# Kernel tuning notes

Measured on AMD Instinct MI355X. Metric: run time of the kernel, lower is better.

Reference implementation:

```python
import jax, jax.numpy as jnp
import numpy as np

ROUTING_ITERS = 3

def squash(t, axis=-1):
    sq_norm = jnp.sum(t * t, axis=axis, keepdims=True)
    scale = sq_norm / (1.0 + sq_norm)
    return scale * t / jnp.sqrt(sq_norm + 1e-8)

def setup_inputs() -> dict:
    key = jax.random.key(0)
    k1, k2 = jax.random.split(key)
    B, N, I, J, O = 64, 2048, 16, 32, 32
    x = jax.random.normal(k1, (B, N, I), dtype=jnp.float32)
    weights = jax.random.normal(k2, (N, J, O, I), dtype=jnp.float32) * 0.1
    return {"x": x, "weights": weights}

def reference(x, weights):
    B, N, _ = x.shape
    J = weights.shape[1]
    # predictions u_{j|i}: [B, N, J, O]
    predictions = jnp.einsum('bni,njoi->bnjo', x, weights)
    b = jnp.zeros((B, N, J, 1), dtype=x.dtype)
    v = None
    for i in range(ROUTING_ITERS):
        c = jax.nn.softmax(b, axis=2)                      # coupling over capsules J
        s = jnp.sum(predictions * c, axis=1, keepdims=True)  # [B,1,J,O]
        v = squash(s, axis=-1)
        if i < ROUTING_ITERS - 1:
            agreement = jnp.sum(predictions * v, axis=-1, keepdims=True)  # [B,N,J,1]
            b = b + agreement
    return jnp.squeeze(v, axis=1)  # [B, J, O]
```

## Files before the change

kernel.cpp:

```cpp
#include <hip/hip_runtime.h>
#include <hip/hip_bf16.h>

#define B_ 64
#define N_ 2048
#define I_ 16
#define J_ 32
#define O_ 32
#define JO_ 1024
#define SPLITS 32

typedef __attribute__((ext_vector_type(8))) short bf16x8;
typedef __attribute__((ext_vector_type(16))) float f32x16;
typedef unsigned short u16;
typedef unsigned int u32;

__device__ __forceinline__ float bf2f(u16 u) {
  union { u32 i; float f; } c; c.i = ((u32)u) << 16; return c.f;
}
__device__ __forceinline__ u16 f2bf(float f) {
  union { float f; u32 i; } c; c.f = f;
  u32 r = (c.i + 0x7fffu + ((c.i >> 16) & 1u)) >> 16;
  return (u16)r;
}
__device__ __forceinline__ u32 pack2_pk(float lo, float hi) {
  u32 r;
  asm("v_cvt_pk_bf16_f32 %0, %1, %2" : "=v"(r) : "v"(lo), "v"(hi));
  return r;
}
__device__ __forceinline__ u32 scale2_pk(u32 p, float cv) {
  union { u32 i; float f; } lo, hi;
  lo.i = p << 16; hi.i = p & 0xffff0000u;
  return pack2_pk(lo.f * cv, hi.f * cv);
}

__global__ __launch_bounds__(256) void xconv_kernel(
    const float* __restrict__ xf, u16* __restrict__ xt)
{
  const int idx = blockIdx.x * 256 + threadIdx.x;
  const int b = idx >> 11, n = idx & 2047;
  const float4* sp = (const float4*)(xf + (size_t)idx * 16);
  float4 f0 = sp[0], f1 = sp[1], f2 = sp[2], f3 = sp[3];
  uint4 d0, d1;
  d0.x = pack2_pk(f0.x, f0.y); d0.y = pack2_pk(f0.z, f0.w);
  d0.z = pack2_pk(f1.x, f1.y); d0.w = pack2_pk(f1.z, f1.w);
  d1.x = pack2_pk(f2.x, f2.y); d1.y = pack2_pk(f2.z, f2.w);
  d1.z = pack2_pk(f3.x, f3.y); d1.w = pack2_pk(f3.z, f3.w);
  uint4* dp = (uint4*)(xt + ((size_t)n * 64 + b) * 16);
  dp[0] = d0; dp[1] = d1;
}

#define SF_NPW 16

__global__ __launch_bounds__(256, 4) void wsf_kernel(
    const float* __restrict__ wf, u16* __restrict__ wb,
    const u16* __restrict__ xt, float* __restrict__ s_part)
{
  __shared__ float red[4][2048];
  const int tid = threadIdx.x;
  const int wave = tid >> 6, lane = tid & 63;
  const int l31 = lane & 31, h = lane >> 5;
  const int j = blockIdx.x, split = blockIdx.y;
  const int n0 = (split * 4 + wave) * SF_NPW;
  f32x16 acc0 = {0.f, 0.f, 0.f, 0.f, 0.f, 0.f, 0.f, 0.f,
                 0.f, 0.f, 0.f, 0.f, 0.f, 0.f, 0.f, 0.f};
  f32x16 acc1 = acc0;

  #pragma unroll 4
  for (int i = 0; i < SF_NPW; ++i) {
    const int n = n0 + i;
    const size_t row = (size_t)n * JO_ + j * 32 + l31;
    const float* wsrc = wf + row * 16 + h * 8;
    const float4 f0 = *(const float4*)(wsrc);
    const float4 f1 = *(const float4*)(wsrc + 4);
    union { uint4 u4; bf16x8 bv; } wd;
    wd.u4.x = pack2_pk(f0.x, f0.y); wd.u4.y = pack2_pk(f0.z, f0.w);
    wd.u4.z = pack2_pk(f1.x, f1.y); wd.u4.w = pack2_pk(f1.z, f1.w);
    *(uint4*)(wb + row * 16 + h * 8) = wd.u4;
    const bf16x8 x0 = *(const bf16x8*)(xt + ((size_t)n * 64 + l31) * 16 + h * 8);
    const bf16x8 x1 = *(const bf16x8*)(xt + ((size_t)n * 64 + 32 + l31) * 16 + h * 8);
    acc0 = __builtin_amdgcn_mfma_f32_32x32x16_bf16(wd.bv, x0, acc0, 0, 0, 0);
    acc1 = __builtin_amdgcn_mfma_f32_32x32x16_bf16(wd.bv, x1, acc1, 0, 0, 0);
  }
  #pragma unroll
  for (int r = 0; r < 16; ++r) {
    const int o = (r & 3) + 8 * (r >> 2) + 4 * h;
    red[wave][o * 64 + l31] = acc0[r];
    red[wave][o * 64 + 32 + l31] = acc1[r];
  }
  __syncthreads();
  float* dst = s_part + (size_t)split * (JO_ * B_) + (size_t)j * 32 * 64;
  #pragma unroll
  for (int k = 0; k < 8; ++k) {
    const int idx = tid + 256 * k;
    dst[idx] = red[0][idx] + red[1][idx] + red[2][idx] + red[3][idx];
  }
}

__global__ __launch_bounds__(256, 4) void sf_kernel(
    const u16* __restrict__ xt, const u16* __restrict__ wb,
    const u16* __restrict__ ct, float* __restrict__ s_part)
{
  __shared__ float red[4][2048];
  const int tid = threadIdx.x;
  const int wave = tid >> 6, lane = tid & 63;
  const int l31 = lane & 31, h = lane >> 5;
  const int j = blockIdx.x, split = blockIdx.y;
  const int n0 = (split * 4 + wave) * SF_NPW;
  f32x16 acc0 = {0.f, 0.f, 0.f, 0.f, 0.f, 0.f, 0.f, 0.f,
                 0.f, 0.f, 0.f, 0.f, 0.f, 0.f, 0.f, 0.f};
  f32x16 acc1 = acc0;

  #pragma unroll 4
  for (int i = 0; i < SF_NPW; ++i) {
    const int n = n0 + i;
    bf16x8 wfr = *(const bf16x8*)(wb + ((size_t)n * JO_ + j * 32 + l31) * 16 + h * 8);
    union { bf16x8 v; u32 u[4]; } a, b2;
    a.v = *(const bf16x8*)(xt + ((size_t)n * 64 + l31) * 16 + h * 8);
    b2.v = *(const bf16x8*)(xt + ((size_t)n * 64 + 32 + l31) * 16 + h * 8);
    const float cv0 = bf2f(ct[((size_t)j * N_ + n) * 64 + l31]);
    const float cv1 = bf2f(ct[((size_t)j * N_ + n) * 64 + 32 + l31]);
    a.u[0] = scale2_pk(a.u[0], cv0); a.u[1] = scale2_pk(a.u[1], cv0);
    a.u[2] = scale2_pk(a.u[2], cv0); a.u[3] = scale2_pk(a.u[3], cv0);
    b2.u[0] = scale2_pk(b2.u[0], cv1); b2.u[1] = scale2_pk(b2.u[1], cv1);
    b2.u[2] = scale2_pk(b2.u[2], cv1); b2.u[3] = scale2_pk(b2.u[3], cv1);
    acc0 = __builtin_amdgcn_mfma_f32_32x32x16_bf16(wfr, a.v, acc0, 0, 0, 0);
    acc1 = __builtin_amdgcn_mfma_f32_32x32x16_bf16(wfr, b2.v, acc1, 0, 0, 0);
  }
  #pragma unroll
  for (int r = 0; r < 16; ++r) {
    const int o = (r & 3) + 8 * (r >> 2) + 4 * h;
    red[wave][o * 64 + l31] = acc0[r];
    red[wave][o * 64 + 32 + l31] = acc1[r];
  }
  __syncthreads();
  float* dst = s_part + (size_t)split * (JO_ * B_) + (size_t)j * 32 * 64;
  #pragma unroll
  for (int k = 0; k < 8; ++k) {
    const int idx = tid + 256 * k;
    dst[idx] = red[0][idx] + red[1][idx] + red[2][idx] + red[3][idx];
  }
}

__global__ __launch_bounds__(64) void r_kernel(
    const float* __restrict__ s_part, float* __restrict__ v,
    const float* __restrict__ vprev, u16* __restrict__ v4,
    float* __restrict__ out, int mode, float scale)
{
  const int tid = threadIdx.x;
  const int jj = tid >> 5, o = tid & 31;
  const int b = blockIdx.x >> 4, jg = blockIdx.x & 15;
  const int j = jg * 2 + jj;
  const size_t off_jo = (size_t)(j * 32 + o) * 64 + b;
  float s = 0.f;
  #pragma unroll
  for (int k = 0; k < SPLITS; ++k) s += s_part[(size_t)k * (JO_ * B_) + off_jo];
  s *= scale;
  float sq = s * s;
  #pragma unroll
  for (int m = 16; m >= 1; m >>= 1) sq += __shfl_xor(sq, m, 64);
  const float sc = sq / (1.f + sq) * rsqrtf(sq + 1e-8f);
  const float vv = sc * s;
  const size_t off = (size_t)b * JO_ + j * 32 + o;
  const int g = o >> 3, hh = (o >> 2) & 1, rr = o & 3;
  const size_t v4off = ((((size_t)j * 4 + g) * 2 + hh) * 64 + b) * 4 + rr;
  if (mode == 0) { v[off] = vv; v4[v4off] = f2bf(vv); }
  else if (mode == 1) { v4[v4off] = f2bf(vv + vprev[off]); }
  else { out[off] = vv; }
}

__global__ __launch_bounds__(256, 6) void a_kernel(
    const u16* __restrict__ xt, const u16* __restrict__ wb,
    const u16* __restrict__ v4, u16* __restrict__ ct)
{
  __shared__ float lgs[64][33];
  const int tid = threadIdx.x;
  const int wave = tid >> 6, lane = tid & 63;
  const int l31 = lane & 31, h = lane >> 5;
  const int n = blockIdx.x;
  const f32x16 zero16 = {0.f, 0.f, 0.f, 0.f, 0.f, 0.f, 0.f, 0.f,
                         0.f, 0.f, 0.f, 0.f, 0.f, 0.f, 0.f, 0.f};

  const bf16x8 x0 = *(const bf16x8*)(xt + ((size_t)n * 64 + l31) * 16 + h * 8);
  const bf16x8 x1 = *(const bf16x8*)(xt + ((size_t)n * 64 + 32 + l31) * 16 + h * 8);

  #pragma unroll 2
  for (int tt = 0; tt < 8; ++tt) {
    const int t = wave * 8 + tt;
    const bf16x8 wfr =
        *(const bf16x8*)(wb + ((size_t)n * JO_ + t * 32 + l31) * 16 + h * 8);
    f32x16 p0 = __builtin_amdgcn_mfma_f32_32x32x16_bf16(wfr, x0, zero16, 0, 0, 0);
    f32x16 p1 = __builtin_amdgcn_mfma_f32_32x32x16_bf16(wfr, x1, zero16, 0, 0, 0);
    float s0 = 0.f, s1 = 0.f;
    #pragma unroll
    for (int g = 0; g < 4; ++g) {
      const int vbase = (((t * 4 + g) * 2 + h) * 64) * 4;
      const ushort4 va = *(const ushort4*)(v4 + vbase + l31 * 4);
      const ushort4 vb = *(const ushort4*)(v4 + vbase + (32 + l31) * 4);
      s0 += p0[g * 4 + 0] * bf2f(va.x) + p0[g * 4 + 1] * bf2f(va.y)
          + p0[g * 4 + 2] * bf2f(va.z) + p0[g * 4 + 3] * bf2f(va.w);
      s1 += p1[g * 4 + 0] * bf2f(vb.x) + p1[g * 4 + 1] * bf2f(vb.y)
          + p1[g * 4 + 2] * bf2f(vb.z) + p1[g * 4 + 3] * bf2f(vb.w);
    }
    s0 += __shfl_xor(s0, 32, 64);
    s1 += __shfl_xor(s1, 32, 64);
    lgs[lane][t] = h ? s1 : s0;
  }
  __syncthreads();

  if (tid < 64) {
    const int b = tid;
    float lv[32];
    float mx = -1e30f;
    #pragma unroll
    for (int t = 0; t < 32; ++t) { lv[t] = lgs[b][t]; mx = fmaxf(mx, lv[t]); }
    float sm = 0.f;
    #pragma unroll
    for (int t = 0; t < 32; ++t) { lv[t] = __expf(lv[t] - mx); sm += lv[t]; }
    const float inv = 1.f / sm;
    #pragma unroll
    for (int t = 0; t < 32; ++t) lgs[b][t] = lv[t] * inv;
  }
  __syncthreads();

  #pragma unroll
  for (int k = 0; k < 8; ++k) {
    const int idx = k * 256 + tid;
    const int t = idx >> 6, b = idx & 63;
    ct[((size_t)t * N_ + n) * 64 + b] = f2bf(lgs[b][t]);
  }
}

extern "C" void kernel_launch(void* const* d_in, const int* in_sizes, int n_in,
                              void* d_out, int out_size, void* d_ws, size_t ws_size,
                              hipStream_t stream) {
  const float* x = (const float*)d_in[0];
  const float* w = (const float*)d_in[1];
  float* out = (float*)d_out;
  char* ws = (char*)d_ws;
  u16*   wb     = (u16*)ws;
  u16*   ct     = (u16*)(ws + (size_t)64 * 1024 * 1024);
  u16*   xt     = (u16*)(ws + (size_t)72 * 1024 * 1024);
  float* s_part = (float*)(ws + (size_t)76 * 1024 * 1024);
  float* v0     = (float*)(ws + (size_t)84 * 1024 * 1024);
  u16*   v4     = (u16*)(ws + (size_t)84 * 1024 * 1024 + 262144);

  dim3 sfg(32, SPLITS), sfb(256);
  dim3 ag(2048), ab(256);
  dim3 rg(1024), rb(64);

  xconv_kernel<<<dim3(512), dim3(256), 0, stream>>>(x, xt);
  wsf_kernel<<<sfg, sfb, 0, stream>>>(w, wb, xt, s_part);
  r_kernel<<<rg, rb, 0, stream>>>(s_part, v0, v0, v4, out, 0, 0.03125f);
  a_kernel<<<ag, ab, 0, stream>>>(xt, wb, v4, ct);
  sf_kernel<<<sfg, sfb, 0, stream>>>(xt, wb, ct, s_part);
  r_kernel<<<rg, rb, 0, stream>>>(s_part, v0, v0, v4, out, 1, 1.0f);
  a_kernel<<<ag, ab, 0, stream>>>(xt, wb, v4, ct);
  sf_kernel<<<sfg, sfb, 0, stream>>>(xt, wb, ct, s_part);
  r_kernel<<<rg, rb, 0, stream>>>(s_part, v0, v0, v4, out, 2, 1.0f);
}
```

Baseline: 331.0 us.

## Fuse agreement, softmax and weighted sum into one per-capsule-set kernel

Replaces the separate agreement/softmax kernel and the weighted-sum kernel with a single kernel. Each block handles 8 input capsules: it computes logits, applies softmax in shared memory, then reuses the same weight and x fragments for the coupled sum. This removes the round trip of the bf16 coupling tensor through global memory and one of the two full passes over the weights per routing iteration. In exchange it writes 256 fp32 partial sums of the full output per iteration. A new reduction kernel then has to read those partials back, which adds substantial memory traffic and an extra launch.

Result: slower. 344.2 us (+4.0%).

```diff
diff --git a/kernel.cpp b/kernel.cpp
--- a/kernel.cpp
+++ b/kernel.cpp
@@ -8,6 +8,8 @@
 #define O_ 32
 #define JO_ 1024
 #define SPLITS 32
+#define ASF_NSET 8
+#define ASF_BLOCKS (N_ / ASF_NSET)
 
 typedef __attribute__((ext_vector_type(8))) short bf16x8;
 typedef __attribute__((ext_vector_type(16))) float f32x16;
@@ -96,53 +98,123 @@
   }
 }
 
-__global__ __launch_bounds__(256, 4) void sf_kernel(
+__global__ __launch_bounds__(512, 2) void asf_kernel(
     const u16* __restrict__ xt, const u16* __restrict__ wb,
-    const u16* __restrict__ ct, float* __restrict__ s_part)
-{
-  __shared__ float red[4][2048];
+    const u16* __restrict__ v4, float* __restrict__ s_part)
+{
+  __shared__ float lgs[ASF_NSET][32][64];
   const int tid = threadIdx.x;
   const int wave = tid >> 6, lane = tid & 63;
   const int l31 = lane & 31, h = lane >> 5;
-  const int j = blockIdx.x, split = blockIdx.y;
-  const int n0 = (split * 4 + wave) * SF_NPW;
-  f32x16 acc0 = {0.f, 0.f, 0.f, 0.f, 0.f, 0.f, 0.f, 0.f,
-                 0.f, 0.f, 0.f, 0.f, 0.f, 0.f, 0.f, 0.f};
-  f32x16 acc1 = acc0;
-
-  #pragma unroll 4
-  for (int i = 0; i < SF_NPW; ++i) {
-    const int n = n0 + i;
-    bf16x8 wfr = *(const bf16x8*)(wb + ((size_t)n * JO_ + j * 32 + l31) * 16 + h * 8);
-    union { bf16x8 v; u32 u[4]; } a, b2;
-    a.v = *(const bf16x8*)(xt + ((size_t)n * 64 + l31) * 16 + h * 8);
-    b2.v = *(const bf16x8*)(xt + ((size_t)n * 64 + 32 + l31) * 16 + h * 8);
-    const float cv0 = bf2f(ct[((size_t)j * N_ + n) * 64 + l31]);
-    const float cv1 = bf2f(ct[((size_t)j * N_ + n) * 64 + 32 + l31]);
-    a.u[0] = scale2_pk(a.u[0], cv0); a.u[1] = scale2_pk(a.u[1], cv0);
-    a.u[2] = scale2_pk(a.u[2], cv0); a.u[3] = scale2_pk(a.u[3], cv0);
-    b2.u[0] = scale2_pk(b2.u[0], cv1); b2.u[1] = scale2_pk(b2.u[1], cv1);
-    b2.u[2] = scale2_pk(b2.u[2], cv1); b2.u[3] = scale2_pk(b2.u[3], cv1);
-    acc0 = __builtin_amdgcn_mfma_f32_32x32x16_bf16(wfr, a.v, acc0, 0, 0, 0);
-    acc1 = __builtin_amdgcn_mfma_f32_32x32x16_bf16(wfr, b2.v, acc1, 0, 0, 0);
-  }
-  #pragma unroll
-  for (int r = 0; r < 16; ++r) {
-    const int o = (r & 3) + 8 * (r >> 2) + 4 * h;
-    red[wave][o * 64 + l31] = acc0[r];
-    red[wave][o * 64 + 32 + l31] = acc1[r];
+  const int nbase = blockIdx.x * ASF_NSET;
+  const f32x16 zero16 = {0.f, 0.f, 0.f, 0.f, 0.f, 0.f, 0.f, 0.f,
+                         0.f, 0.f, 0.f, 0.f, 0.f, 0.f, 0.f, 0.f};
+
+  for (int nn = 0; nn < ASF_NSET; ++nn) {
+    const int n = nbase + nn;
+    const bf16x8 x0 = *(const bf16x8*)(xt + ((size_t)n * 64 + l31) * 16 + h * 8);
+    const bf16x8 x1 = *(const bf16x8*)(xt + ((size_t)n * 64 + 32 + l31) * 16 + h * 8);
+    #pragma unroll 2
+    for (int q = 0; q < 4; ++q) {
+      const int t = wave * 4 + q;
+      const bf16x8 wfr =
+          *(const bf16x8*)(wb + ((size_t)n * JO_ + t * 32 + l31) * 16 + h * 8);
+      f32x16 p0 = __builtin_amdgcn_mfma_f32_32x32x16_bf16(wfr, x0, zero16, 0, 0, 0);
+      f32x16 p1 = __builtin_amdgcn_mfma_f32_32x32x16_bf16(wfr, x1, zero16, 0, 0, 0);
+      float s0 = 0.f, s1 = 0.f;
+      #pragma unroll
+      for (int g = 0; g < 4; ++g) {
+        const int vbase = (((t * 4 + g) * 2 + h) * 64) * 4;
+        const ushort4 va = *(const ushort4*)(v4 + vbase + l31 * 4);
+        const ushort4 vb = *(const ushort4*)(v4 + vbase + (32 + l31) * 4);
+        s0 += p0[g * 4 + 0] * bf2f(va.x) + p0[g * 4 + 1] * bf2f(va.y)
+            + p0[g * 4 + 2] * bf2f(va.z) + p0[g * 4 + 3] * bf2f(va.w);
+        s1 += p1[g * 4 + 0] * bf2f(vb.x) + p1[g * 4 + 1] * bf2f(vb.y)
+            + p1[g * 4 + 2] * bf2f(vb.z) + p1[g * 4 + 3] * bf2f(vb.w);
+      }
+      s0 += __shfl_xor(s0, 32, 64);
+      s1 += __shfl_xor(s1, 32, 64);
+      lgs[nn][t][lane] = h ? s1 : s0;
+    }
   }
   __syncthreads();
-  float* dst = s_part + (size_t)split * (JO_ * B_) + (size_t)j * 32 * 64;
-  #pragma unroll
-  for (int k = 0; k < 8; ++k) {
-    const int idx = tid + 256 * k;
-    dst[idx] = red[0][idx] + red[1][idx] + red[2][idx] + red[3][idx];
-  }
+
+  {
+    const int n2 = tid >> 6, b = tid & 63;
+    float lv[32];
+    float mx = -1e30f;
+    #pragma unroll
+    for (int t = 0; t < 32; ++t) { lv[t] = lgs[n2][t][b]; mx = fmaxf(mx, lv[t]); }
+    float sm = 0.f;
+    #pragma unroll
+    for (int t = 0; t < 32; ++t) { lv[t] = __expf(lv[t] - mx); sm += lv[t]; }
+    const float inv = 1.f / sm;
+    #pragma unroll
+    for (int t = 0; t < 32; ++t) lgs[n2][t][b] = lv[t] * inv;
+  }
+  __syncthreads();
+
+  f32x16 a0_0 = zero16, a0_1 = zero16, a0_2 = zero16, a0_3 = zero16;
+  f32x16 a1_0 = zero16, a1_1 = zero16, a1_2 = zero16, a1_3 = zero16;
+  for (int nn = 0; nn < ASF_NSET; ++nn) {
+    const int n = nbase + nn;
+    union { bf16x8 v; u32 u[4]; } xa, xb;
+    xa.v = *(const bf16x8*)(xt + ((size_t)n * 64 + l31) * 16 + h * 8);
+    xb.v = *(const bf16x8*)(xt + ((size_t)n * 64 + 32 + l31) * 16 + h * 8);
+    #pragma unroll
+    for (int q = 0; q < 4; ++q) {
+      const int t = wave * 4 + q;
+      const bf16x8 wfr =
+          *(const bf16x8*)(wb + ((size_t)n * JO_ + t * 32 + l31) * 16 + h * 8);
+      const float cv0 = lgs[nn][t][l31];
+      const float cv1 = lgs[nn][t][32 + l31];
+      union { bf16x8 v; u32 u[4]; } s0, s1;
+      s0.u[0] = scale2_pk(xa.u[0], cv0); s0.u[1] = scale2_pk(xa.u[1], cv0);
+      s0.u[2] = scale2_pk(xa.u[2], cv0); s0.u[3] = scale2_pk(xa.u[3], cv0);
+      s1.u[0] = scale2_pk(xb.u[0], cv1); s1.u[1] = scale2_pk(xb.u[1], cv1);
+      s1.u[2] = scale2_pk(xb.u[2], cv1); s1.u[3] = scale2_pk(xb.u[3], cv1);
+      if (q == 0) {
+        a0_0 = __builtin_amdgcn_mfma_f32_32x32x16_bf16(wfr, s0.v, a0_0, 0, 0, 0);
+        a1_0 = __builtin_amdgcn_mfma_f32_32x32x16_bf16(wfr, s1.v, a1_0, 0, 0, 0);
+      } else if (q == 1) {
+        a0_1 = __builtin_amdgcn_mfma_f32_32x32x16_bf16(wfr, s0.v, a0_1, 0, 0, 0);
+        a1_1 = __builtin_amdgcn_mfma_f32_32x32x16_bf16(wfr, s1.v, a1_1, 0, 0, 0);
+      } else if (q == 2) {
+        a0_2 = __builtin_amdgcn_mfma_f32_32x32x16_bf16(wfr, s0.v, a0_2, 0, 0, 0);
+        a1_2 = __builtin_amdgcn_mfma_f32_32x32x16_bf16(wfr, s1.v, a1_2, 0, 0, 0);
+      } else {
+        a0_3 = __builtin_amdgcn_mfma_f32_32x32x16_bf16(wfr, s0.v, a0_3, 0, 0, 0);
+        a1_3 = __builtin_amdgcn_mfma_f32_32x32x16_bf16(wfr, s1.v, a1_3, 0, 0, 0);
+      }
+    }
+  }
+  float* dst = s_part + (size_t)blockIdx.x * (JO_ * B_);
+  #pragma unroll
+  for (int q = 0; q < 4; ++q) {
+    const int t = wave * 4 + q;
+    const f32x16 a0 = (q == 0) ? a0_0 : (q == 1) ? a0_1 : (q == 2) ? a0_2 : a0_3;
+    const f32x16 a1 = (q == 0) ? a1_0 : (q == 1) ? a1_1 : (q == 2) ? a1_2 : a1_3;
+    #pragma unroll
+    for (int r = 0; r < 16; ++r) {
+      const int o = (r & 3) + 8 * (r >> 2) + 4 * h;
+      dst[(size_t)(t * 32 + o) * 64 + l31] = a0[r];
+      dst[(size_t)(t * 32 + o) * 64 + 32 + l31] = a1[r];
+    }
+  }
+}
+
+__global__ __launch_bounds__(256) void rs_kernel(
+    const float* __restrict__ src, float* __restrict__ dst, int nsplit)
+{
+  const int idx = blockIdx.x * 256 + threadIdx.x;
+  float s = 0.f;
+  #pragma unroll 8
+  for (int p = 0; p < nsplit; ++p) s += src[(size_t)p * (JO_ * B_) + idx];
+  dst[idx] = s;
 }
 
 __global__ __launch_bounds__(64) void r_kernel(
-    const float* __restrict__ s_part, float* __restrict__ v,
+    const float* __restrict__ s_red, float* __restrict__ v,
     const float* __restrict__ vprev, u16* __restrict__ v4,
     float* __restrict__ out, int mode, float scale)
 {
@@ -150,11 +222,7 @@
   const int jj = tid >> 5, o = tid & 31;
   const int b = blockIdx.x >> 4, jg = blockIdx.x & 15;
   const int j = jg * 2 + jj;
-  const size_t off_jo = (size_t)(j * 32 + o) * 64 + b;
-  float s = 0.f;
-  #pragma unroll
-  for (int k = 0; k < SPLITS; ++k) s += s_part[(size_t)k * (JO_ * B_) + off_jo];
-  s *= scale;
+  const float s = s_red[(size_t)(j * 32 + o) * 64 + b] * scale;
   float sq = s * s;
   #pragma unroll
   for (int m = 16; m >= 1; m >>= 1) sq += __shfl_xor(sq, m, 64);
@@ -168,68 +236,6 @@
   else { out[off] = vv; }
 }
 
-__global__ __launch_bounds__(256, 6) void a_kernel(
-    const u16* __restrict__ xt, const u16* __restrict__ wb,
-    const u16* __restrict__ v4, u16* __restrict__ ct)
-{
-  __shared__ float lgs[64][33];
-  const int tid = threadIdx.x;
-  const int wave = tid >> 6, lane = tid & 63;
-  const int l31 = lane & 31, h = lane >> 5;
-  const int n = blockIdx.x;
-  const f32x16 zero16 = {0.f, 0.f, 0.f, 0.f, 0.f, 0.f, 0.f, 0.f,
-                         0.f, 0.f, 0.f, 0.f, 0.f, 0.f, 0.f, 0.f};
-
-  const bf16x8 x0 = *(const bf16x8*)(xt + ((size_t)n * 64 + l31) * 16 + h * 8);
-  const bf16x8 x1 = *(const bf16x8*)(xt + ((size_t)n * 64 + 32 + l31) * 16 + h * 8);
-
-  #pragma unroll 2
-  for (int tt = 0; tt < 8; ++tt) {
-    const int t = wave * 8 + tt;
-    const bf16x8 wfr =
-        *(const bf16x8*)(wb + ((size_t)n * JO_ + t * 32 + l31) * 16 + h * 8);
-    f32x16 p0 = __builtin_amdgcn_mfma_f32_32x32x16_bf16(wfr, x0, zero16, 0, 0, 0);
-    f32x16 p1 = __builtin_amdgcn_mfma_f32_32x32x16_bf16(wfr, x1, zero16, 0, 0, 0);
-    float s0 = 0.f, s1 = 0.f;
-    #pragma unroll
-    for (int g = 0; g < 4; ++g) {
-      const int vbase = (((t * 4 + g) * 2 + h) * 64) * 4;
-      const ushort4 va = *(const ushort4*)(v4 + vbase + l31 * 4);
-      const ushort4 vb = *(const ushort4*)(v4 + vbase + (32 + l31) * 4);
-      s0 += p0[g * 4 + 0] * bf2f(va.x) + p0[g * 4 + 1] * bf2f(va.y)
-          + p0[g * 4 + 2] * bf2f(va.z) + p0[g * 4 + 3] * bf2f(va.w);
-      s1 += p1[g * 4 + 0] * bf2f(vb.x) + p1[g * 4 + 1] * bf2f(vb.y)
-          + p1[g * 4 + 2] * bf2f(vb.z) + p1[g * 4 + 3] * bf2f(vb.w);
-    }
-    s0 += __shfl_xor(s0, 32, 64);
-    s1 += __shfl_xor(s1, 32, 64);
-    lgs[lane][t] = h ? s1 : s0;
-  }
-  __syncthreads();
-
-  if (tid < 64) {
-    const int b = tid;
-    float lv[32];
-    float mx = -1e30f;
-    #pragma unroll
-    for (int t = 0; t < 32; ++t) { lv[t] = lgs[b][t]; mx = fmaxf(mx, lv[t]); }
-    float sm = 0.f;
-    #pragma unroll
-    for (int t = 0; t < 32; ++t) { lv[t] = __expf(lv[t] - mx); sm += lv[t]; }
-    const float inv = 1.f / sm;
-    #pragma unroll
-    for (int t = 0; t < 32; ++t) lgs[b][t] = lv[t] * inv;
-  }
-  __syncthreads();
-
-  #pragma unroll
-  for (int k = 0; k < 8; ++k) {
-    const int idx = k * 256 + tid;
-    const int t = idx >> 6, b = idx & 63;
-    ct[((size_t)t * N_ + n) * 64 + b] = f2bf(lgs[b][t]);
-  }
-}
-
 extern "C" void kernel_launch(void* const* d_in, const int* in_sizes, int n_in,
                               void* d_out, int out_size, void* d_ws, size_t ws_size,
                               hipStream_t stream) {
@@ -237,24 +243,27 @@
   const float* w = (const float*)d_in[1];
   float* out = (float*)d_out;
   char* ws = (char*)d_ws;
-  u16*   wb     = (u16*)ws;
-  u16*   ct     = (u16*)(ws + (size_t)64 * 1024 * 1024);
-  u16*   xt     = (u16*)(ws + (size_t)72 * 1024 * 1024);
-  float* s_part = (float*)(ws + (size_t)76 * 1024 * 1024);
-  float* v0     = (float*)(ws + (size_t)84 * 1024 * 1024);
-  u16*   v4     = (u16*)(ws + (size_t)84 * 1024 * 1024 + 262144);
+  u16*   wb       = (u16*)ws;
+  u16*   xt       = (u16*)(ws + (size_t)64 * 1024 * 1024);
+  float* s_part32 = (float*)(ws + (size_t)68 * 1024 * 1024);
+  float* s_red    = (float*)(ws + (size_t)76 * 1024 * 1024);
+  float* v0       = (float*)(ws + (size_t)76 * 1024 * 1024 + 262144);
+  u16*   v4       = (u16*)(ws + (size_t)76 * 1024 * 1024 + 2 * 262144);
+  float* s_partA  = (float*)(ws + (size_t)80 * 1024 * 1024);
 
   dim3 sfg(32, SPLITS), sfb(256);
-  dim3 ag(2048), ab(256);
+  dim3 ag(ASF_BLOCKS), ab(512);
+  dim3 rsg(256), rsb(256);
   dim3 rg(1024), rb(64);
 
   xconv_kernel<<<dim3(512), dim3(256), 0, stream>>>(x, xt);
-  wsf_kernel<<<sfg, sfb, 0, stream>>>(w, wb, xt, s_part);
-  r_kernel<<<rg, rb, 0, stream>>>(s_part, v0, v0, v4, out, 0, 0.03125f);
-  a_kernel<<<ag, ab, 0, stream>>>(xt, wb, v4, ct);
-  sf_kernel<<<sfg, sfb, 0, stream>>>(xt, wb, ct, s_part);
-  r_kernel<<<rg, rb, 0, stream>>>(s_part, v0, v0, v4, out, 1, 1.0f);
-  a_kernel<<<ag, ab, 0, stream>>>(xt, wb, v4, ct);
-  sf_kernel<<<sfg, sfb, 0, stream>>>(xt, wb, ct, s_part);
-  r_kernel<<<rg, rb, 0, stream>>>(s_part, v0, v0, v4, out, 2, 1.0f);
-}
+  wsf_kernel<<<sfg, sfb, 0, stream>>>(w, wb, xt, s_part32);
+  rs_kernel<<<rsg, rsb, 0, stream>>>(s_part32, s_red, SPLITS);
+  r_kernel<<<rg, rb, 0, stream>>>(s_red, v0, v0, v4, out, 0, 0.03125f);
+  asf_kernel<<<ag, ab, 0, stream>>>(xt, wb, v4, s_partA);
+  rs_kernel<<<rsg, rsb, 0, stream>>>(s_partA, s_red, ASF_BLOCKS);
+  r_kernel<<<rg, rb, 0, stream>>>(s_red, v0, v0, v4, out, 1, 1.0f);
+  asf_kernel<<<ag, ab, 0, stream>>>(xt, wb, v4, s_partA);
+  rs_kernel<<<rsg, rsb, 0, stream>>>(s_partA, s_red, ASF_BLOCKS);
+  r_kernel<<<rg, rb, 0, stream>>>(s_red, v0, v0, v4, out, 2, 1.0f);
+}
```

## Software-pipeline sf/a loads, double sf splits, add coalesced split-reduction kernel

Applied to the files above, without the earlier changes.

The sf kernel now uses 64 splits of 8 rows each and prefetches the next row's W, x and coupling values one iteration ahead. The agreement kernel gets the same prefetch, and the v4 layout is reorganised so each lane reads 16 contiguous bf16 values as two uint4 loads. The split-partial summation moves out of r_kernel into a separate coalesced rs_kernel. The goal is to hide load latency and raise parallelism, at the cost of more partial-sum traffic and three extra launches.

Result: slower. 904.3 us (+173.2%).

```diff
diff --git a/kernel.cpp b/kernel.cpp
--- a/kernel.cpp
+++ b/kernel.cpp
@@ -7,7 +7,8 @@
 #define J_ 32
 #define O_ 32
 #define JO_ 1024
-#define SPLITS 32
+#define WSPLITS 32
+#define SFSPLITS 64
 
 typedef __attribute__((ext_vector_type(8))) short bf16x8;
 typedef __attribute__((ext_vector_type(16))) float f32x16;
@@ -31,6 +32,17 @@
   union { u32 i; float f; } lo, hi;
   lo.i = p << 16; hi.i = p & 0xffff0000u;
   return pack2_pk(lo.f * cv, hi.f * cv);
+}
+__device__ __forceinline__ float dot16(const f32x16& p, uint4 lo, uint4 hi) {
+  const u32 w[8] = {lo.x, lo.y, lo.z, lo.w, hi.x, hi.y, hi.z, hi.w};
+  float s = 0.f;
+  #pragma unroll
+  for (int k = 0; k < 8; ++k) {
+    union { u32 i; float f; } a, b;
+    a.i = w[k] << 16; b.i = w[k] & 0xffff0000u;
+    s += p[2 * k] * a.f + p[2 * k + 1] * b.f;
+  }
+  return s;
 }
 
 __global__ __launch_bounds__(256) void xconv_kernel(
@@ -49,7 +61,7 @@
   dp[0] = d0; dp[1] = d1;
 }
 
-#define SF_NPW 16
+#define WSF_NPW 16
 
 __global__ __launch_bounds__(256, 4) void wsf_kernel(
     const float* __restrict__ wf, u16* __restrict__ wb,
@@ -60,13 +72,13 @@
   const int wave = tid >> 6, lane = tid & 63;
   const int l31 = lane & 31, h = lane >> 5;
   const int j = blockIdx.x, split = blockIdx.y;
-  const int n0 = (split * 4 + wave) * SF_NPW;
+  const int n0 = (split * 4 + wave) * WSF_NPW;
   f32x16 acc0 = {0.f, 0.f, 0.f, 0.f, 0.f, 0.f, 0.f, 0.f,
                  0.f, 0.f, 0.f, 0.f, 0.f, 0.f, 0.f, 0.f};
   f32x16 acc1 = acc0;
 
   #pragma unroll 4
-  for (int i = 0; i < SF_NPW; ++i) {
+  for (int i = 0; i < WSF_NPW; ++i) {
     const int n = n0 + i;
     const size_t row = (size_t)n * JO_ + j * 32 + l31;
     const float* wsrc = wf + row * 16 + h * 8;
@@ -96,6 +108,8 @@
   }
 }
 
+#define SF_NPW 8
+
 __global__ __launch_bounds__(256, 4) void sf_kernel(
     const u16* __restrict__ xt, const u16* __restrict__ wb,
     const u16* __restrict__ ct, float* __restrict__ s_part)
@@ -110,21 +124,35 @@
                  0.f, 0.f, 0.f, 0.f, 0.f, 0.f, 0.f, 0.f};
   f32x16 acc1 = acc0;
 
-  #pragma unroll 4
+  bf16x8 wfr = *(const bf16x8*)(wb + ((size_t)n0 * JO_ + j * 32 + l31) * 16 + h * 8);
+  union { bf16x8 v; u32 u[4]; } xa, xb;
+  xa.v = *(const bf16x8*)(xt + ((size_t)n0 * 64 + l31) * 16 + h * 8);
+  xb.v = *(const bf16x8*)(xt + ((size_t)n0 * 64 + 32 + l31) * 16 + h * 8);
+  float cv0 = bf2f(ct[((size_t)j * N_ + n0) * 64 + l31]);
+  float cv1 = bf2f(ct[((size_t)j * N_ + n0) * 64 + 32 + l31]);
+
+  #pragma unroll
   for (int i = 0; i < SF_NPW; ++i) {
-    const int n = n0 + i;
-    bf16x8 wfr = *(const bf16x8*)(wb + ((size_t)n * JO_ + j * 32 + l31) * 16 + h * 8);
-    union { bf16x8 v; u32 u[4]; } a, b2;
-    a.v = *(const bf16x8*)(xt + ((size_t)n * 64 + l31) * 16 + h * 8);
-    b2.v = *(const bf16x8*)(xt + ((size_t)n * 64 + 32 + l31) * 16 + h * 8);
-    const float cv0 = bf2f(ct[((size_t)j * N_ + n) * 64 + l31]);
-    const float cv1 = bf2f(ct[((size_t)j * N_ + n) * 64 + 32 + l31]);
-    a.u[0] = scale2_pk(a.u[0], cv0); a.u[1] = scale2_pk(a.u[1], cv0);
-    a.u[2] = scale2_pk(a.u[2], cv0); a.u[3] = scale2_pk(a.u[3], cv0);
-    b2.u[0] = scale2_pk(b2.u[0], cv1); b2.u[1] = scale2_pk(b2.u[1], cv1);
-    b2.u[2] = scale2_pk(b2.u[2], cv1); b2.u[3] = scale2_pk(b2.u[3], cv1);
-    acc0 = __builtin_amdgcn_mfma_f32_32x32x16_bf16(wfr, a.v, acc0, 0, 0, 0);
-    acc1 = __builtin_amdgcn_mfma_f32_32x32x16_bf16(wfr, b2.v, acc1, 0, 0, 0);
+    bf16x8 wfr_n = wfr;
+    union { bf16x8 v; u32 u[4]; } xa_n, xb_n;
+    xa_n.v = xa.v; xb_n.v = xb.v;
+    float c0n = cv0, c1n = cv1;
+    if (i + 1 < SF_NPW) {
+      const int n1 = n0 + i + 1;
+      wfr_n = *(const bf16x8*)(wb + ((size_t)n1 * JO_ + j * 32 + l31) * 16 + h * 8);
+      xa_n.v = *(const bf16x8*)(xt + ((size_t)n1 * 64 + l31) * 16 + h * 8);
+      xb_n.v = *(const bf16x8*)(xt + ((size_t)n1 * 64 + 32 + l31) * 16 + h * 8);
+      c0n = bf2f(ct[((size_t)j * N_ + n1) * 64 + l31]);
+      c1n = bf2f(ct[((size_t)j * N_ + n1) * 64 + 32 + l31]);
+    }
+    union { bf16x8 v; u32 u[4]; } s0, s1;
+    s0.u[0] = scale2_pk(xa.u[0], cv0); s0.u[1] = scale2_pk(xa.u[1], cv0);
+    s0.u[2] = scale2_pk(xa.u[2], cv0); s0.u[3] = scale2_pk(xa.u[3], cv0);
+    s1.u[0] = scale2_pk(xb.u[0], cv1); s1.u[1] = scale2_pk(xb.u[1], cv1);
+    s1.u[2] = scale2_pk(xb.u[2], cv1); s1.u[3] = scale2_pk(xb.u[3], cv1);
+    acc0 = __builtin_amdgcn_mfma_f32_32x32x16_bf16(wfr, s0.v, acc0, 0, 0, 0);
+    acc1 = __builtin_amdgcn_mfma_f32_32x32x16_bf16(wfr, s1.v, acc1, 0, 0, 0);
+    wfr = wfr_n; xa.v = xa_n.v; xb.v = xb_n.v; cv0 = c0n; cv1 = c1n;
   }
   #pragma unroll
   for (int r = 0; r < 16; ++r) {
@@ -141,8 +169,18 @@
   }
 }
 
+__global__ __launch_bounds__(256) void rs_kernel(
+    const float* __restrict__ src, float* __restrict__ dst, int nsplit)
+{
+  const int idx = blockIdx.x * 256 + threadIdx.x;
+  float s = 0.f;
+  #pragma unroll 8
+  for (int p = 0; p < nsplit; ++p) s += src[(size_t)p * (JO_ * B_) + idx];
+  dst[idx] = s;
+}
+
 __global__ __launch_bounds__(64) void r_kernel(
-    const float* __restrict__ s_part, float* __restrict__ v,
+    const float* __restrict__ s_red, float* __restrict__ v,
     const float* __restrict__ vprev, u16* __restrict__ v4,
     float* __restrict__ out, int mode, float scale)
 {
@@ -150,11 +188,7 @@
   const int jj = tid >> 5, o = tid & 31;
   const int b = blockIdx.x >> 4, jg = blockIdx.x & 15;
   const int j = jg * 2 + jj;
-  const size_t off_jo = (size_t)(j * 32 + o) * 64 + b;
-  float s = 0.f;
-  #pragma unroll
-  for (int k = 0; k < SPLITS; ++k) s += s_part[(size_t)k * (JO_ * B_) + off_jo];
-  s *= scale;
+  const float s = s_red[(size_t)(j * 32 + o) * 64 + b] * scale;
   float sq = s * s;
   #pragma unroll
   for (int m = 16; m >= 1; m >>= 1) sq += __shfl_xor(sq, m, 64);
@@ -162,7 +196,7 @@
   const float vv = sc * s;
   const size_t off = (size_t)b * JO_ + j * 32 + o;
   const int g = o >> 3, hh = (o >> 2) & 1, rr = o & 3;
-  const size_t v4off = ((((size_t)j * 4 + g) * 2 + hh) * 64 + b) * 4 + rr;
+  const size_t v4off = (((size_t)j * 2 + hh) * 64 + b) * 16 + g * 4 + rr;
   if (mode == 0) { v[off] = vv; v4[v4off] = f2bf(vv); }
   else if (mode == 1) { v4[v4off] = f2bf(vv + vprev[off]); }
   else { out[off] = vv; }
@@ -183,27 +217,36 @@
   const bf16x8 x0 = *(const bf16x8*)(xt + ((size_t)n * 64 + l31) * 16 + h * 8);
   const bf16x8 x1 = *(const bf16x8*)(xt + ((size_t)n * 64 + 32 + l31) * 16 + h * 8);
 
-  #pragma unroll 2
-  for (int tt = 0; tt < 8; ++tt) {
-    const int t = wave * 8 + tt;
-    const bf16x8 wfr =
-        *(const bf16x8*)(wb + ((size_t)n * JO_ + t * 32 + l31) * 16 + h * 8);
-    f32x16 p0 = __builtin_amdgcn_mfma_f32_32x32x16_bf16(wfr, x0, zero16, 0, 0, 0);
-    f32x16 p1 = __builtin_amdgcn_mfma_f32_32x32x16_bf16(wfr, x1, zero16, 0, 0, 0);
-    float s0 = 0.f, s1 = 0.f;
+  {
+    const int t0 = wave * 8;
+    bf16x8 wfr = *(const bf16x8*)(wb + ((size_t)n * JO_ + t0 * 32 + l31) * 16 + h * 8);
+    const u16* pa = v4 + (((size_t)t0 * 2 + h) * 64 + l31) * 16;
+    const u16* pb = v4 + (((size_t)t0 * 2 + h) * 64 + 32 + l31) * 16;
+    uint4 va0 = *(const uint4*)(pa), va1 = *(const uint4*)(pa + 8);
+    uint4 vb0 = *(const uint4*)(pb), vb1 = *(const uint4*)(pb + 8);
+
     #pragma unroll
-    for (int g = 0; g < 4; ++g) {
-      const int vbase = (((t * 4 + g) * 2 + h) * 64) * 4;
-      const ushort4 va = *(const ushort4*)(v4 + vbase + l31 * 4);
-      const ushort4 vb = *(const ushort4*)(v4 + vbase + (32 + l31) * 4);
-      s0 += p0[g * 4 + 0] * bf2f(va.x) + p0[g * 4 + 1] * bf2f(va.y)
-          + p0[g * 4 + 2] * bf2f(va.z) + p0[g * 4 + 3] * bf2f(va.w);
-      s1 += p1[g * 4 + 0] * bf2f(vb.x) + p1[g * 4 + 1] * bf2f(vb.y)
-          + p1[g * 4 + 2] * bf2f(vb.z) + p1[g * 4 + 3] * bf2f(vb.w);
+    for (int tt = 0; tt < 8; ++tt) {
+      const int t = wave * 8 + tt;
+      bf16x8 wfr_n = wfr;
+      uint4 va0n = va0, va1n = va1, vb0n = vb0, vb1n = vb1;
+      if (tt + 1 < 8) {
+        const int t1 = t + 1;
+        wfr_n = *(const bf16x8*)(wb + ((size_t)n * JO_ + t1 * 32 + l31) * 16 + h * 8);
+        const u16* qa = v4 + (((size_t)t1 * 2 + h) * 64 + l31) * 16;
+        const u16* qb = v4 + (((size_t)t1 * 2 + h) * 64 + 32 + l31) * 16;
+        va0n = *(const uint4*)(qa); va1n = *(const uint4*)(qa + 8);
+        vb0n = *(const uint4*)(qb); vb1n = *(const uint4*)(qb + 8);
+      }
+      f32x16 p0 = __builtin_amdgcn_mfma_f32_32x32x16_bf16(wfr, x0, zero16, 0, 0, 0);
+      f32x16 p1 = __builtin_amdgcn_mfma_f32_32x32x16_bf16(wfr, x1, zero16, 0, 0, 0);
+      float s0 = dot16(p0, va0, va1);
+      float s1 = dot16(p1, vb0, vb1);
+      s0 += __shfl_xor(s0, 32, 64);
+      s1 += __shfl_xor(s1, 32, 64);
+      lgs[lane][t] = h ? s1 : s0;
+      wfr = wfr_n; va0 = va0n; va1 = va1n; vb0 = vb0n; vb1 = vb1n;
     }
-    s0 += __shfl_xor(s0, 32, 64);
-    s1 += __shfl_xor(s1, 32, 64);
-    lgs[lane][t] = h ? s1 : s0;
   }
   __syncthreads();
 
@@ -237,24 +280,31 @@
   const float* w = (const float*)d_in[1];
   float* out = (float*)d_out;
   char* ws = (char*)d_ws;
-  u16*   wb     = (u16*)ws;
-  u16*   ct     = (u16*)(ws + (size_t)64 * 1024 * 1024);
-  u16*   xt     = (u16*)(ws + (size_t)72 * 1024 * 1024);
-  float* s_part = (float*)(ws + (size_t)76 * 1024 * 1024);
-  float* v0     = (float*)(ws + (size_t)84 * 1024 * 1024);
-  u16*   v4     = (u16*)(ws + (size_t)84 * 1024 * 1024 + 262144);
-
-  dim3 sfg(32, SPLITS), sfb(256);
+  u16*   wb       = (u16*)ws;
+  u16*   xt       = (u16*)(ws + (size_t)64 * 1024 * 1024);
+  float* s_part32 = (float*)(ws + (size_t)68 * 1024 * 1024);
+  float* s_red    = (float*)(ws + (size_t)76 * 1024 * 1024);
+  float* v0       = (float*)(ws + (size_t)76 * 1024 * 1024 + 262144);
+  u16*   v4       = (u16*)(ws + (size_t)76 * 1024 * 1024 + 2 * 262144);
+  u16*   ct       = (u16*)(ws + (size_t)78 * 1024 * 1024);
+  float* s_partSF = (float*)(ws + (size_t)88 * 1024 * 1024);
+
+  dim3 wsfg(32, WSPLITS), wsfb(256);
+  dim3 sfg(32, SFSPLITS), sfb(256);
   dim3 ag(2048), ab(256);
+  dim3 rsg(256), rsb(256);
   dim3 rg(1024), rb(64);
 
   xconv_kernel<<<dim3(512), dim3(256), 0, stream>>>(x, xt);
-  wsf_kernel<<<sfg, sfb, 0, stream>>>(w, wb, xt, s_part);
-  r_kernel<<<rg, rb, 0, stream>>>(s_part, v0, v0, v4, out, 0, 0.03125f);
+  wsf_kernel<<<wsfg, wsfb, 0, stream>>>(w, wb, xt, s_part32);
+  rs_kernel<<<rsg, rsb, 0, stream>>>(s_part32, s_red, WSPLITS);
+  r_kernel<<<rg, rb, 0, stream>>>(s_red, v0, v0, v4, out, 0, 0.03125f);
   a_kernel<<<ag, ab, 0, stream>>>(xt, wb, v4, ct);
-  sf_kernel<<<sfg, sfb, 0, stream>>>(xt, wb, ct, s_part);
-  r_kernel<<<rg, rb, 0, stream>>>(s_part, v0, v0, v4, out, 1, 1.0f);
+  sf_kernel<<<sfg, sfb, 0, stream>>>(xt, wb, ct, s_partSF);
+  rs_kernel<<<rsg, rsb, 0, stream>>>(s_partSF, s_red, SFSPLITS);
+  r_kernel<<<rg, rb, 0, stream>>>(s_red, v0, v0, v4, out, 1, 1.0f);
   a_kernel<<<ag, ab, 0, stream>>>(xt, wb, v4, ct);
-  sf_kernel<<<sfg, sfb, 0, stream>>>(xt, wb, ct, s_part);
-  r_kernel<<<rg, rb, 0, stream>>>(s_part, v0, v0, v4, out, 2, 1.0f);
-}
+  sf_kernel<<<sfg, sfb, 0, stream>>>(xt, wb, ct, s_partSF);
+  rs_kernel<<<rsg, rsb, 0, stream>>>(s_partSF, s_red, SFSPLITS);
+  r_kernel<<<rg, rb, 0, stream>>>(s_red, v0, v0, v4, out, 2, 1.0f);
+}
```
